# Kernel tuning notes

Hardware: AMD Instinct MI355X
Metric: run time of the kernel (lower is better)

The kernel has to match this reference:

```python
import jax, jax.numpy as jnp
import numpy as np

N, C, H = 4096, 1024, 16
HD = C // H            # 64
DR = HD // 8           # 8 rope freqs per spatial axis


def setup_inputs() -> dict:
    key = jax.random.key(0)
    k1, k2, k3, k4, k5, k6 = jax.random.split(key, 6)
    x = jax.random.normal(k1, (N, C), dtype=jnp.float32)
    coords = jax.random.randint(k2, (N, 5), 0, 64, dtype=jnp.int32)  # [batch, t, h, w, z]
    w_qkv = jax.random.normal(k3, (3 * C, C), dtype=jnp.float32) / np.sqrt(C)
    w_out = jax.random.normal(k4, (C, C), dtype=jnp.float32) / np.sqrt(C)
    gamma_q = jnp.ones((H, HD), dtype=jnp.float32)
    gamma_k = jnp.ones((H, HD), dtype=jnp.float32)
    return {"x": x, "coords": coords, "w_qkv": w_qkv, "w_out": w_out,
            "gamma_q": gamma_q, "gamma_k": gamma_k}


def _rms_norm(t, gamma):
    # F.normalize(dim=-1) * gamma * sqrt(head_dim), computed in fp32
    t = t.astype(jnp.float32)
    nrm = jnp.linalg.norm(t, axis=-1, keepdims=True)
    return t / jnp.maximum(nrm, 1e-12) * gamma * np.float32(np.sqrt(HD))


def _rope_angles(coords):
    # freqs = 1/10000^(arange(DR)/HD); angles per axis (t,h,w,z), concat -> [N, 4*DR] = [N, HD/2]
    freqs = 1.0 / (10000.0 ** (jnp.arange(DR, dtype=jnp.float32) / HD))
    pos = coords[:, 1:].astype(jnp.float32)  # [N,4]
    ang = pos[:, :, None] * freqs[None, None, :]  # [N,4,DR]
    return ang.reshape(ang.shape[0], -1)  # [N, HD/2]


def _apply_rope(t, cos, sin):
    # t: [N,H,HD]; pairs (2i, 2i+1) rotated by angle[i]
    t2 = t.astype(jnp.float32).reshape(t.shape[0], t.shape[1], -1, 2)
    re = t2[..., 0] * cos - t2[..., 1] * sin
    im = t2[..., 0] * sin + t2[..., 1] * cos
    return jnp.stack([re, im], axis=-1).reshape(t.shape)


def reference(x, coords, w_qkv, w_out, gamma_q, gamma_k):
    n = x.shape[0]
    qkv = (x @ w_qkv.T).reshape(n, 3, H, HD)
    q, k, v = qkv[:, 0], qkv[:, 1], qkv[:, 2]  # [N,H,HD]
    q = _rms_norm(q, gamma_q)
    k = _rms_norm(k, gamma_k)
    ang = _rope_angles(coords)              # [N, HD/2]
    cos = jnp.cos(ang)[:, None, :]          # [N,1,HD/2] (broadcast over heads)
    sin = jnp.sin(ang)[:, None, :]
    q = _apply_rope(q, cos, sin)
    k = _apply_rope(k, cos, sin)
    scale = np.float32(1.0 / np.sqrt(HD))
    scores = jnp.einsum('nhd,mhd->hnm', q, k) * scale  # [H,N,N]
    attn = jax.nn.softmax(scores, axis=-1)
    out = jnp.einsum('hnm,mhd->nhd', attn, v).reshape(n, C)
    return out @ w_out.T
```

## Files before the change

kernel.cpp:

```cpp
#include <hip/hip_runtime.h>
#include <hip/hip_bf16.h>

typedef _Float16 half8 __attribute__((ext_vector_type(8)));
typedef _Float16 half4v __attribute__((ext_vector_type(4)));
typedef _Float16 half2 __attribute__((ext_vector_type(2)));
typedef float f32x4 __attribute__((ext_vector_type(4)));

constexpr int NT = 4096;
constexpr int CH = 1024;
constexpr int NH = 16;
constexpr int HD = 64;
constexpr int C3 = 3072;

#if __has_builtin(__builtin_amdgcn_exp2f)
#define EXP2(x) __builtin_amdgcn_exp2f(x)
#else
#define EXP2(x) exp2f(x)
#endif

#define GLOAD_LDS16(gp, lp) __builtin_amdgcn_global_load_lds( \
    (const __attribute__((address_space(1))) void*)(gp),      \
    (__attribute__((address_space(3))) void*)(lp), 16, 0, 0)

static __device__ inline half2 pk_f16(float a, float b) {
  auto r = __builtin_amdgcn_cvt_pkrtz(a, b);
  return *(half2*)&r;
}

__global__ __launch_bounds__(256) void cvt_kernel(const float* __restrict__ in,
                                                  _Float16* __restrict__ out, int n4) {
  int i = blockIdx.x * 256 + threadIdx.x;
  if (i >= n4) return;
  float4 v = ((const float4*)in)[i];
  half4v h;
  h[0] = (_Float16)v.x; h[1] = (_Float16)v.y; h[2] = (_Float16)v.z; h[3] = (_Float16)v.w;
  ((half4v*)out)[i] = h;
}

template <typename OutT>
__global__ __launch_bounds__(256) void gemm_bt(const _Float16* __restrict__ A,
                                               const _Float16* __restrict__ Bt,
                                               OutT* __restrict__ Cc,
                                               int M, int Nn, int K) {
  __shared__ _Float16 As[2][128][32];
  __shared__ _Float16 Bs[2][128][32];
  const int tid = threadIdx.x;
  const int lane = tid & 63, w = tid >> 6;
  const int l15 = lane & 15, l4 = lane >> 4;
  const int m0 = blockIdx.x * 128, n0 = blockIdx.y * 128;
  const int wr = w >> 1, wc = w & 1;
  const int rb = w * 32;
  const int rl = lane >> 2;
  const int cb = (lane & 3) * 8;
  f32x4 acc[4][4] = {};
  auto stage = [&](int k0, int buf) {
    GLOAD_LDS16(A  + (size_t)(m0 + rb + rl) * K + k0 + cb,      &As[buf][rb][0]);
    GLOAD_LDS16(A  + (size_t)(m0 + rb + 16 + rl) * K + k0 + cb, &As[buf][rb + 16][0]);
    GLOAD_LDS16(Bt + (size_t)(n0 + rb + rl) * K + k0 + cb,      &Bs[buf][rb][0]);
    GLOAD_LDS16(Bt + (size_t)(n0 + rb + 16 + rl) * K + k0 + cb, &Bs[buf][rb + 16][0]);
  };
  auto compute = [&](int buf) {
    half8 af[4], bf[4];
#pragma unroll
    for (int mt = 0; mt < 4; ++mt) af[mt] = *(half8*)&As[buf][wr * 64 + mt * 16 + l15][l4 * 8];
#pragma unroll
    for (int nt = 0; nt < 4; ++nt) bf[nt] = *(half8*)&Bs[buf][wc * 64 + nt * 16 + l15][l4 * 8];
#pragma unroll
    for (int mt = 0; mt < 4; ++mt)
#pragma unroll
      for (int nt = 0; nt < 4; ++nt)
        acc[mt][nt] = __builtin_amdgcn_mfma_f32_16x16x32_f16(af[mt], bf[nt], acc[mt][nt], 0, 0, 0);
  };
  stage(0, 0);
  __syncthreads();
  for (int k0 = 0; k0 < K; k0 += 64) {
    stage(k0 + 32, 1);
    compute(0);
    __syncthreads();
    if (k0 + 64 < K) stage(k0 + 64, 0);
    compute(1);
    __syncthreads();
  }
#pragma unroll
  for (int mt = 0; mt < 4; ++mt)
#pragma unroll
    for (int nt = 0; nt < 4; ++nt)
#pragma unroll
      for (int r = 0; r < 4; ++r) {
        int row = m0 + wr * 64 + mt * 16 + l4 * 4 + r;
        int col = n0 + wc * 64 + nt * 16 + l15;
        Cc[(size_t)row * Nn + col] = (OutT)acc[mt][nt][r];
      }
}

__global__ __launch_bounds__(256) void rmsrope_kernel(const _Float16* __restrict__ qkv,
                                                      const int* __restrict__ coords,
                                                      const float* __restrict__ gq,
                                                      const float* __restrict__ gk,
                                                      _Float16* __restrict__ Qh,
                                                      _Float16* __restrict__ KF) {
  int gw = blockIdx.x * 4 + (threadIdx.x >> 6);
  int lane = threadIdx.x & 63;
  int n = gw >> 4, h = gw & 15;
  float q = (float)qkv[(size_t)n * C3 + h * HD + lane];
  float k = (float)qkv[(size_t)n * C3 + CH + h * HD + lane];
  float sq = q * q, sk = k * k;
#pragma unroll
  for (int m = 1; m < 64; m <<= 1) { sq += __shfl_xor(sq, m); sk += __shfl_xor(sk, m); }
  q *= 8.0f / fmaxf(sqrtf(sq), 1e-12f) * gq[h * HD + lane];
  k *= 8.0f / fmaxf(sqrtf(sk), 1e-12f) * gk[h * HD + lane];
  int j = lane >> 1, p = j >> 3, dr = j & 7;
  float ang = (float)coords[n * 5 + 1 + p] * __expf(-(float)dr * 0.14391157f);
  float cs = cosf(ang), sn = sinf(ang);
  float qp = __shfl_xor(q, 1), kp = __shfl_xor(k, 1);
  float qr, kr;
  if ((lane & 1) == 0) { qr = q * cs - qp * sn; kr = k * cs - kp * sn; }
  else                 { qr = qp * sn + q * cs; kr = kp * sn + k * cs; }
  Qh[((size_t)h * NT + n) * HD + lane] = (_Float16)(qr * 0.18033688f);
  int m64 = n & 63, kb = n >> 6;
  int t   = 2 * (m64 >> 5) + ((m64 >> 2) & 1);
  int i15 = 4 * ((m64 >> 3) & 3) + (m64 & 3);
  int kk = lane >> 5, ll4 = (lane >> 3) & 3, jj = lane & 7;
  KF[(size_t)h * NT * HD + (size_t)kb * 4096 +
     (size_t)(((t * 2 + kk) * 64 + ll4 * 16 + i15) * 8 + jj)] = (_Float16)kr;
}

__global__ __launch_bounds__(256) void vtrans_kernel(const _Float16* __restrict__ qkv,
                                                     _Float16* __restrict__ VF) {
  __shared__ _Float16 L[64][72];
  int h = blockIdx.y, n0 = blockIdx.x * 64, kb = blockIdx.x, t0 = threadIdx.x;
#pragma unroll
  for (int i = 0; i < 2; ++i) {
    int cid = t0 + i * 256, r = cid >> 3, c = cid & 7;
    *(half8*)&L[r][c * 8] = *(const half8*)(qkv + (size_t)(n0 + r) * C3 + 2 * CH + h * HD + c * 8);
  }
  __syncthreads();
#pragma unroll
  for (int i = 0; i < 2; ++i) {
    int cid = t0 + i * 256, d = cid >> 3, c = cid & 7;
    half8 v;
#pragma unroll
    for (int jj = 0; jj < 8; ++jj) v[jj] = L[c * 8 + jj][d];
    size_t flat = (size_t)h * NT * HD + (size_t)kb * 4096 +
                  (size_t)((((d >> 4) * 2 + (c >> 2)) * 64 + (c & 3) * 16 + (d & 15)) * 8);
    *(half8*)(VF + flat) = v;
  }
}

__global__ __launch_bounds__(256, 2) void attn_kernel(const _Float16* __restrict__ Qh,
                                                      const _Float16* __restrict__ KF,
                                                      const _Float16* __restrict__ VF,
                                                      _Float16* __restrict__ Oh) {
  __shared__ _Float16 KB[2][4096];
  __shared__ _Float16 VB[2][4096];
  const int tid = threadIdx.x, lane = tid & 63, w = tid >> 6;
  const int l15 = lane & 15, l4 = lane >> 4;
  int bid = blockIdx.x;
  int s = bid >> 3;
  int h = (bid & 7) * 2 + (s >> 5);
  int n0 = (s & 31) * 128;
  half8 qf[2][2];
#pragma unroll
  for (int qb = 0; qb < 2; ++qb)
#pragma unroll
    for (int kk = 0; kk < 2; ++kk)
      qf[qb][kk] = *(const half8*)(Qh + ((size_t)h * NT + n0 + w * 32 + qb * 16 + l15) * HD + kk * 32 + l4 * 8);
  f32x4 acc[2][4] = {};
  f32x4 acc5[2] = {};
  half8 of1 = {};
  if (l15 == 0) {
#pragma unroll
    for (int jq = 0; jq < 8; ++jq) of1[jq] = (_Float16)1.0f;
  }
  const _Float16* KFh = KF + (size_t)h * NT * HD + w * 512 + lane * 8;
  const _Float16* VFh = VF + (size_t)h * NT * HD + w * 512 + lane * 8;
  union U { half8 v; half2 p[4]; };
  auto stage = [&](int kb, int buf) {
    size_t g0 = (size_t)kb * 4096;
    GLOAD_LDS16(KFh + g0,        &KB[buf][w * 512]);
    GLOAD_LDS16(KFh + g0 + 2048, &KB[buf][2048 + w * 512]);
    GLOAD_LDS16(VFh + g0,        &VB[buf][w * 512]);
    GLOAD_LDS16(VFh + g0 + 2048, &VB[buf][2048 + w * 512]);
  };
  auto compute = [&](int buf) {
    f32x4 sv[2][4] = {};
    __builtin_amdgcn_s_setprio(1);
#pragma unroll
    for (int t = 0; t < 4; ++t)
#pragma unroll
      for (int kk = 0; kk < 2; ++kk) {
        half8 kf = *(half8*)&KB[buf][(t * 2 + kk) * 512 + lane * 8];
        sv[0][t] = __builtin_amdgcn_mfma_f32_16x16x32_f16(kf, qf[0][kk], sv[0][t], 0, 0, 0);
        sv[1][t] = __builtin_amdgcn_mfma_f32_16x16x32_f16(kf, qf[1][kk], sv[1][t], 0, 0, 0);
      }
    __builtin_amdgcn_s_setprio(0);
    U u[2][2];
#pragma unroll
    for (int qb = 0; qb < 2; ++qb) {
      float e[4][4];
#pragma unroll
      for (int t = 0; t < 4; ++t)
#pragma unroll
        for (int r = 0; r < 4; ++r) e[t][r] = EXP2(sv[qb][t][r]);
      u[qb][0].p[0] = pk_f16(e[0][0], e[0][1]); u[qb][0].p[1] = pk_f16(e[0][2], e[0][3]);
      u[qb][0].p[2] = pk_f16(e[1][0], e[1][1]); u[qb][0].p[3] = pk_f16(e[1][2], e[1][3]);
      u[qb][1].p[0] = pk_f16(e[2][0], e[2][1]); u[qb][1].p[1] = pk_f16(e[2][2], e[2][3]);
      u[qb][1].p[2] = pk_f16(e[3][0], e[3][1]); u[qb][1].p[3] = pk_f16(e[3][2], e[3][3]);
    }
    __builtin_amdgcn_s_setprio(1);
#pragma unroll
    for (int t = 0; t < 4; ++t)
#pragma unroll
      for (int kk = 0; kk < 2; ++kk) {
        half8 vf = *(half8*)&VB[buf][(t * 2 + kk) * 512 + lane * 8];
        acc[0][t] = __builtin_amdgcn_mfma_f32_16x16x32_f16(u[0][kk].v, vf, acc[0][t], 0, 0, 0);
        acc[1][t] = __builtin_amdgcn_mfma_f32_16x16x32_f16(u[1][kk].v, vf, acc[1][t], 0, 0, 0);
      }
    acc5[0] = __builtin_amdgcn_mfma_f32_16x16x32_f16(u[0][0].v, of1, acc5[0], 0, 0, 0);
    acc5[0] = __builtin_amdgcn_mfma_f32_16x16x32_f16(u[0][1].v, of1, acc5[0], 0, 0, 0);
    acc5[1] = __builtin_amdgcn_mfma_f32_16x16x32_f16(u[1][0].v, of1, acc5[1], 0, 0, 0);
    acc5[1] = __builtin_amdgcn_mfma_f32_16x16x32_f16(u[1][1].v, of1, acc5[1], 0, 0, 0);
    __builtin_amdgcn_s_setprio(0);
  };
  stage(0, 0);
  __syncthreads();
  for (int kb = 0; kb < 64; kb += 2) {
    stage(kb + 1, 1);
    compute(0);
    __syncthreads();
    if (kb + 2 < 64) stage(kb + 2, 0);
    compute(1);
    __syncthreads();
  }
#pragma unroll
  for (int qb = 0; qb < 2; ++qb) {
    float linv[4];
#pragma unroll
    for (int r = 0; r < 4; ++r) linv[r] = 1.0f / __shfl(acc5[qb][r], lane & 48);
#pragma unroll
    for (int t = 0; t < 4; ++t)
#pragma unroll
      for (int r = 0; r < 4; ++r) {
        int row = n0 + w * 32 + qb * 16 + l4 * 4 + r;
        Oh[(size_t)row * CH + h * HD + t * 16 + l15] = (_Float16)(acc[qb][t][r] * linv[r]);
      }
  }
}

extern "C" void kernel_launch(void* const* d_in, const int* in_sizes, int n_in,
                              void* d_out, int out_size, void* d_ws, size_t ws_size,
                              hipStream_t stream) {
  const float* x      = (const float*)d_in[0];
  const int*   coords = (const int*)d_in[1];
  const float* w_qkv  = (const float*)d_in[2];
  const float* w_out  = (const float*)d_in[3];
  const float* gq     = (const float*)d_in[4];
  const float* gk     = (const float*)d_in[5];
  float* out = (float*)d_out;

  char* ws = (char*)d_ws;
  size_t off = 0;
  auto alloc = [&](size_t bytes) { char* p = ws + off; off += bytes; return p; };
  _Float16* xh   = (_Float16*)alloc((size_t)NT * CH * 2);
  _Float16* wqh  = (_Float16*)alloc((size_t)C3 * CH * 2);
  _Float16* woh  = (_Float16*)alloc((size_t)CH * CH * 2);
  _Float16* qkvh = (_Float16*)alloc((size_t)NT * C3 * 2);
  _Float16* Qh   = (_Float16*)alloc((size_t)NT * CH * 2);
  _Float16* KFh  = (_Float16*)alloc((size_t)NT * CH * 2);
  _Float16* VFh  = (_Float16*)alloc((size_t)NT * CH * 2);
  _Float16* Oh   = (_Float16*)alloc((size_t)NT * CH * 2);
  if (off > ws_size) return;

  cvt_kernel<<<NT * CH / 4 / 256, 256, 0, stream>>>(x, xh, NT * CH / 4);
  cvt_kernel<<<C3 * CH / 4 / 256, 256, 0, stream>>>(w_qkv, wqh, C3 * CH / 4);
  cvt_kernel<<<CH * CH / 4 / 256, 256, 0, stream>>>(w_out, woh, CH * CH / 4);
  gemm_bt<_Float16><<<dim3(NT / 128, C3 / 128), 256, 0, stream>>>(xh, wqh, qkvh, NT, C3, CH);
  rmsrope_kernel<<<NT * NH / 4, 256, 0, stream>>>(qkvh, coords, gq, gk, Qh, KFh);
  vtrans_kernel<<<dim3(NT / 64, NH), 256, 0, stream>>>(qkvh, VFh);
  attn_kernel<<<NH * (NT / 128), 256, 0, stream>>>(Qh, KFh, VFh, Oh);
  gemm_bt<float><<<dim3(NT / 128, CH / 128), 256, 0, stream>>>(Oh, woh, out, NT, CH, CH);
}
```

Measured before the change: 177.6 us.

## Fuse conversions, remap GEMM blocks across XCDs, widen attention per-wave query tile

The three fp32-to-fp16 conversion launches are merged into one kernel. Both GEMMs switch to a 1D grid whose block IDs are remapped so consecutive tiles land on the same XCD, aiming at better L2 reuse. The attention kernel drops to 128 threads with 2 waves, and each wave now handles 64 query rows instead of 32, so every K/V fragment read from LDS feeds twice as many MFMAs. This raises register pressure (launch bounds 128,1) and halves the waves per block, which risks lower latency hiding and occupancy.

```diff
diff --git a/kernel.cpp b/kernel.cpp
--- a/kernel.cpp
+++ b/kernel.cpp
@@ -27,27 +27,37 @@
   return *(half2*)&r;
 }
 
-__global__ __launch_bounds__(256) void cvt_kernel(const float* __restrict__ in,
-                                                  _Float16* __restrict__ out, int n4) {
+__global__ __launch_bounds__(256) void cvt3_kernel(const float* __restrict__ a, int na4,
+                                                   const float* __restrict__ b, int nb4,
+                                                   const float* __restrict__ c, int nc4,
+                                                   _Float16* __restrict__ oa,
+                                                   _Float16* __restrict__ ob,
+                                                   _Float16* __restrict__ oc) {
   int i = blockIdx.x * 256 + threadIdx.x;
-  if (i >= n4) return;
-  float4 v = ((const float4*)in)[i];
+  const float* src; _Float16* dst; int j = i;
+  if (i < na4) { src = a; dst = oa; }
+  else if (i < na4 + nb4) { src = b; dst = ob; j = i - na4; }
+  else if (i < na4 + nb4 + nc4) { src = c; dst = oc; j = i - na4 - nb4; }
+  else return;
+  float4 v = ((const float4*)src)[j];
   half4v h;
   h[0] = (_Float16)v.x; h[1] = (_Float16)v.y; h[2] = (_Float16)v.z; h[3] = (_Float16)v.w;
-  ((half4v*)out)[i] = h;
+  ((half4v*)dst)[j] = h;
 }
 
 template <typename OutT>
 __global__ __launch_bounds__(256) void gemm_bt(const _Float16* __restrict__ A,
                                                const _Float16* __restrict__ Bt,
                                                OutT* __restrict__ Cc,
-                                               int M, int Nn, int K) {
+                                               int M, int Nn, int K, int nbx) {
   __shared__ _Float16 As[2][128][32];
   __shared__ _Float16 Bs[2][128][32];
   const int tid = threadIdx.x;
   const int lane = tid & 63, w = tid >> 6;
   const int l15 = lane & 15, l4 = lane >> 4;
-  const int m0 = blockIdx.x * 128, n0 = blockIdx.y * 128;
+  int nwg = gridDim.x, cpx = nwg >> 3;
+  int wg = (blockIdx.x & 7) * cpx + (blockIdx.x >> 3);
+  const int m0 = (wg % nbx) * 128, n0 = (wg / nbx) * 128;
   const int wr = w >> 1, wc = w & 1;
   const int rb = w * 32;
   const int rl = lane >> 2;
@@ -147,7 +157,7 @@
   }
 }
 
-__global__ __launch_bounds__(256, 2) void attn_kernel(const _Float16* __restrict__ Qh,
+__global__ __launch_bounds__(128, 1) void attn_kernel(const _Float16* __restrict__ Qh,
                                                       const _Float16* __restrict__ KF,
                                                       const _Float16* __restrict__ VF,
                                                       _Float16* __restrict__ Oh) {
@@ -159,44 +169,46 @@
   int s = bid >> 3;
   int h = (bid & 7) * 2 + (s >> 5);
   int n0 = (s & 31) * 128;
-  half8 qf[2][2];
-#pragma unroll
-  for (int qb = 0; qb < 2; ++qb)
+  half8 qf[4][2];
+#pragma unroll
+  for (int qb = 0; qb < 4; ++qb)
 #pragma unroll
     for (int kk = 0; kk < 2; ++kk)
-      qf[qb][kk] = *(const half8*)(Qh + ((size_t)h * NT + n0 + w * 32 + qb * 16 + l15) * HD + kk * 32 + l4 * 8);
-  f32x4 acc[2][4] = {};
-  f32x4 acc5[2] = {};
+      qf[qb][kk] = *(const half8*)(Qh + ((size_t)h * NT + n0 + w * 64 + qb * 16 + l15) * HD + kk * 32 + l4 * 8);
+  f32x4 acc[4][4] = {};
+  f32x4 acc5[4] = {};
   half8 of1 = {};
   if (l15 == 0) {
 #pragma unroll
     for (int jq = 0; jq < 8; ++jq) of1[jq] = (_Float16)1.0f;
   }
-  const _Float16* KFh = KF + (size_t)h * NT * HD + w * 512 + lane * 8;
-  const _Float16* VFh = VF + (size_t)h * NT * HD + w * 512 + lane * 8;
+  const _Float16* KFh = KF + (size_t)h * NT * HD + w * 2048 + lane * 8;
+  const _Float16* VFh = VF + (size_t)h * NT * HD + w * 2048 + lane * 8;
   union U { half8 v; half2 p[4]; };
   auto stage = [&](int kb, int buf) {
     size_t g0 = (size_t)kb * 4096;
-    GLOAD_LDS16(KFh + g0,        &KB[buf][w * 512]);
-    GLOAD_LDS16(KFh + g0 + 2048, &KB[buf][2048 + w * 512]);
-    GLOAD_LDS16(VFh + g0,        &VB[buf][w * 512]);
-    GLOAD_LDS16(VFh + g0 + 2048, &VB[buf][2048 + w * 512]);
+#pragma unroll
+    for (int g = 0; g < 4; ++g) {
+      GLOAD_LDS16(KFh + g0 + g * 512, &KB[buf][w * 2048 + g * 512]);
+      GLOAD_LDS16(VFh + g0 + g * 512, &VB[buf][w * 2048 + g * 512]);
+    }
   };
   auto compute = [&](int buf) {
-    f32x4 sv[2][4] = {};
+    f32x4 sv[4][4] = {};
     __builtin_amdgcn_s_setprio(1);
 #pragma unroll
     for (int t = 0; t < 4; ++t)
 #pragma unroll
       for (int kk = 0; kk < 2; ++kk) {
         half8 kf = *(half8*)&KB[buf][(t * 2 + kk) * 512 + lane * 8];
-        sv[0][t] = __builtin_amdgcn_mfma_f32_16x16x32_f16(kf, qf[0][kk], sv[0][t], 0, 0, 0);
-        sv[1][t] = __builtin_amdgcn_mfma_f32_16x16x32_f16(kf, qf[1][kk], sv[1][t], 0, 0, 0);
+#pragma unroll
+        for (int qb = 0; qb < 4; ++qb)
+          sv[qb][t] = __builtin_amdgcn_mfma_f32_16x16x32_f16(kf, qf[qb][kk], sv[qb][t], 0, 0, 0);
       }
     __builtin_amdgcn_s_setprio(0);
-    U u[2][2];
-#pragma unroll
-    for (int qb = 0; qb < 2; ++qb) {
+    U u[4][2];
+#pragma unroll
+    for (int qb = 0; qb < 4; ++qb) {
       float e[4][4];
 #pragma unroll
       for (int t = 0; t < 4; ++t)
@@ -213,13 +225,15 @@
 #pragma unroll
       for (int kk = 0; kk < 2; ++kk) {
         half8 vf = *(half8*)&VB[buf][(t * 2 + kk) * 512 + lane * 8];
-        acc[0][t] = __builtin_amdgcn_mfma_f32_16x16x32_f16(u[0][kk].v, vf, acc[0][t], 0, 0, 0);
-        acc[1][t] = __builtin_amdgcn_mfma_f32_16x16x32_f16(u[1][kk].v, vf, acc[1][t], 0, 0, 0);
-      }
-    acc5[0] = __builtin_amdgcn_mfma_f32_16x16x32_f16(u[0][0].v, of1, acc5[0], 0, 0, 0);
-    acc5[0] = __builtin_amdgcn_mfma_f32_16x16x32_f16(u[0][1].v, of1, acc5[0], 0, 0, 0);
-    acc5[1] = __builtin_amdgcn_mfma_f32_16x16x32_f16(u[1][0].v, of1, acc5[1], 0, 0, 0);
-    acc5[1] = __builtin_amdgcn_mfma_f32_16x16x32_f16(u[1][1].v, of1, acc5[1], 0, 0, 0);
+#pragma unroll
+        for (int qb = 0; qb < 4; ++qb)
+          acc[qb][t] = __builtin_amdgcn_mfma_f32_16x16x32_f16(u[qb][kk].v, vf, acc[qb][t], 0, 0, 0);
+      }
+#pragma unroll
+    for (int qb = 0; qb < 4; ++qb) {
+      acc5[qb] = __builtin_amdgcn_mfma_f32_16x16x32_f16(u[qb][0].v, of1, acc5[qb], 0, 0, 0);
+      acc5[qb] = __builtin_amdgcn_mfma_f32_16x16x32_f16(u[qb][1].v, of1, acc5[qb], 0, 0, 0);
+    }
     __builtin_amdgcn_s_setprio(0);
   };
   stage(0, 0);
@@ -233,7 +247,7 @@
     __syncthreads();
   }
 #pragma unroll
-  for (int qb = 0; qb < 2; ++qb) {
+  for (int qb = 0; qb < 4; ++qb) {
     float linv[4];
 #pragma unroll
     for (int r = 0; r < 4; ++r) linv[r] = 1.0f / __shfl(acc5[qb][r], lane & 48);
@@ -241,7 +255,7 @@
     for (int t = 0; t < 4; ++t)
 #pragma unroll
       for (int r = 0; r < 4; ++r) {
-        int row = n0 + w * 32 + qb * 16 + l4 * 4 + r;
+        int row = n0 + w * 64 + qb * 16 + l4 * 4 + r;
         Oh[(size_t)row * CH + h * HD + t * 16 + l15] = (_Float16)(acc[qb][t][r] * linv[r]);
       }
   }
@@ -271,12 +285,12 @@
   _Float16* Oh   = (_Float16*)alloc((size_t)NT * CH * 2);
   if (off > ws_size) return;
 
-  cvt_kernel<<<NT * CH / 4 / 256, 256, 0, stream>>>(x, xh, NT * CH / 4);
-  cvt_kernel<<<C3 * CH / 4 / 256, 256, 0, stream>>>(w_qkv, wqh, C3 * CH / 4);
-  cvt_kernel<<<CH * CH / 4 / 256, 256, 0, stream>>>(w_out, woh, CH * CH / 4);
-  gemm_bt<_Float16><<<dim3(NT / 128, C3 / 128), 256, 0, stream>>>(xh, wqh, qkvh, NT, C3, CH);
+  int na4 = NT * CH / 4, nb4 = C3 * CH / 4, nc4 = CH * CH / 4;
+  cvt3_kernel<<<(na4 + nb4 + nc4) / 256, 256, 0, stream>>>(x, na4, w_qkv, nb4, w_out, nc4,
+                                                           xh, wqh, woh);
+  gemm_bt<_Float16><<<(NT / 128) * (C3 / 128), 256, 0, stream>>>(xh, wqh, qkvh, NT, C3, CH, NT / 128);
   rmsrope_kernel<<<NT * NH / 4, 256, 0, stream>>>(qkvh, coords, gq, gk, Qh, KFh);
   vtrans_kernel<<<dim3(NT / 64, NH), 256, 0, stream>>>(qkvh, VFh);
-  attn_kernel<<<NH * (NT / 128), 256, 0, stream>>>(Qh, KFh, VFh, Oh);
-  gemm_bt<float><<<dim3(NT / 128, CH / 128), 256, 0, stream>>>(Oh, woh, out, NT, CH, CH);
-}
+  attn_kernel<<<NH * (NT / 128), 128, 0, stream>>>(Qh, KFh, VFh, Oh);
+  gemm_bt<float><<<(NT / 128) * (CH / 128), 256, 0, stream>>>(Oh, woh, out, NT, CH, CH, NT / 128);
+}
```

After: 196.8 us. 10.8% more time.

## Add 256x256 fragment-layout QKV GEMM, XCD-swizzle blocks, single-buffer attention

Applied to the files above, without the earlier changes.

Converts x and w_qkv into a pre-tiled fragment layout so a new 512-thread 256x256-tile GEMM can stage whole K-tiles with direct global-to-LDS loads and interleave prefetch with MFMA phases. It also remaps workgroup IDs so neighbouring tiles land on the same XCD, in both GEMMs. The attention kernel drops its K/V double buffer for a single buffer with two barriers per step, which lowers LDS use but exposes load latency. The new GEMM requests 128KB of dynamic LDS at two blocks per CU, which depends on the LDS capacity available.

```diff
diff --git a/kernel.cpp b/kernel.cpp
--- a/kernel.cpp
+++ b/kernel.cpp
@@ -37,17 +37,117 @@
   ((half4v*)out)[i] = h;
 }
 
+__global__ __launch_bounds__(256) void cvt_frag_kernel(const float* __restrict__ in,
+                                                       _Float16* __restrict__ out,
+                                                       int n4, int Kd) {
+  int i = blockIdx.x * 256 + threadIdx.x;
+  if (i >= n4) return;
+  int kq = Kd >> 2;
+  int r = i / kq, k = (i - r * kq) * 4;
+  float4 v = ((const float4*)in)[i];
+  int bt = r >> 8, rr = r & 255;
+  int kt = k >> 6, kr = k & 63;
+  int frag = ((rr >> 4) << 1) + (kr >> 5);
+  size_t flat = (((size_t)bt * (Kd >> 6) + kt) * 32 + frag) * 512
+              + ((((kr >> 3) & 3) * 16 + (rr & 15)) << 3) + (kr & 7);
+  half4v h;
+  h[0] = (_Float16)v.x; h[1] = (_Float16)v.y; h[2] = (_Float16)v.z; h[3] = (_Float16)v.w;
+  *(half4v*)(out + flat) = h;
+}
+
+__global__ __launch_bounds__(512, 2) void gemm8p(const _Float16* __restrict__ A2,
+                                                 const _Float16* __restrict__ B2,
+                                                 _Float16* __restrict__ Cc,
+                                                 int M, int Nn, int K, int nbx) {
+  extern __shared__ _Float16 lds[];
+  const int tid = threadIdx.x;
+  const int lane = tid & 63, w = tid >> 6;
+  const int l15 = lane & 15, l4 = lane >> 4;
+  const int wr = w >> 2, wc = w & 3;
+  int nwg = gridDim.x, cpx = nwg >> 3;
+  int wg = (blockIdx.x & 7) * cpx + (blockIdx.x >> 3);
+  const int bm = wg % nbx, bn = wg / nbx;
+  const int ktiles = K >> 6;
+  const _Float16* Abase = A2 + (size_t)bm * ktiles * 16384 + tid * 8;
+  const _Float16* Bbase = B2 + (size_t)bn * ktiles * 16384 + tid * 8;
+  f32x4 acc[8][4] = {};
+  auto stageA = [&](int kt, int buf) {
+    const _Float16* s = Abase + (size_t)kt * 16384;
+    _Float16* d = lds + buf * 16384 + tid * 8;
+#pragma unroll
+    for (int i = 0; i < 4; ++i) GLOAD_LDS16(s + i * 4096, d + i * 4096);
+  };
+  auto stageB = [&](int kt, int buf) {
+    const _Float16* s = Bbase + (size_t)kt * 16384;
+    _Float16* d = lds + 32768 + buf * 16384 + tid * 8;
+#pragma unroll
+    for (int i = 0; i < 4; ++i) GLOAD_LDS16(s + i * 4096, d + i * 4096);
+  };
+  stageA(0, 0);
+  stageB(0, 0);
+  for (int kt = 0; kt < ktiles; ++kt) {
+    const int cur = kt & 1, nxt = cur ^ 1;
+    const _Float16* Ac = lds + cur * 16384 + lane * 8;
+    const _Float16* Bc = lds + 32768 + cur * 16384 + lane * 8;
+    asm volatile("s_waitcnt vmcnt(0)" ::: "memory");
+    __builtin_amdgcn_sched_barrier(0);
+    __builtin_amdgcn_s_barrier();
+    __builtin_amdgcn_sched_barrier(0);
+#pragma unroll
+    for (int ph = 0; ph < 4; ++ph) {
+      const int mh = ph >> 1, nh = ph & 1;
+      half8 af[4][2], bf[2][2];
+#pragma unroll
+      for (int mt = 0; mt < 4; ++mt)
+#pragma unroll
+        for (int kk = 0; kk < 2; ++kk)
+          af[mt][kk] = *(half8*)(Ac + ((((wr * 8 + mh * 4 + mt) << 1) + kk) << 9));
+#pragma unroll
+      for (int nt = 0; nt < 2; ++nt)
+#pragma unroll
+        for (int kk = 0; kk < 2; ++kk)
+          bf[nt][kk] = *(half8*)(Bc + ((((wc * 4 + nh * 2 + nt) << 1) + kk) << 9));
+      if (ph == 0 && kt + 1 < ktiles) stageA(kt + 1, nxt);
+      if (ph == 1 && kt + 1 < ktiles) stageB(kt + 1, nxt);
+      __builtin_amdgcn_s_barrier();
+      __builtin_amdgcn_s_setprio(1);
+#pragma unroll
+      for (int mt = 0; mt < 4; ++mt)
+#pragma unroll
+        for (int nt = 0; nt < 2; ++nt)
+#pragma unroll
+          for (int kk = 0; kk < 2; ++kk)
+            acc[mh * 4 + mt][nh * 2 + nt] = __builtin_amdgcn_mfma_f32_16x16x32_f16(
+                af[mt][kk], bf[nt][kk], acc[mh * 4 + mt][nh * 2 + nt], 0, 0, 0);
+      __builtin_amdgcn_s_setprio(0);
+      __builtin_amdgcn_s_barrier();
+    }
+  }
+#pragma unroll
+  for (int mt8 = 0; mt8 < 8; ++mt8)
+#pragma unroll
+    for (int nt4 = 0; nt4 < 4; ++nt4)
+#pragma unroll
+      for (int r = 0; r < 4; ++r) {
+        int row = bm * 256 + wr * 128 + mt8 * 16 + l4 * 4 + r;
+        int col = bn * 256 + wc * 64 + nt4 * 16 + l15;
+        Cc[(size_t)row * Nn + col] = (_Float16)acc[mt8][nt4][r];
+      }
+}
+
 template <typename OutT>
 __global__ __launch_bounds__(256) void gemm_bt(const _Float16* __restrict__ A,
                                                const _Float16* __restrict__ Bt,
                                                OutT* __restrict__ Cc,
-                                               int M, int Nn, int K) {
+                                               int M, int Nn, int K, int nbx) {
   __shared__ _Float16 As[2][128][32];
   __shared__ _Float16 Bs[2][128][32];
   const int tid = threadIdx.x;
   const int lane = tid & 63, w = tid >> 6;
   const int l15 = lane & 15, l4 = lane >> 4;
-  const int m0 = blockIdx.x * 128, n0 = blockIdx.y * 128;
+  int nwg = gridDim.x, cpx = nwg >> 3;
+  int wg = (blockIdx.x & 7) * cpx + (blockIdx.x >> 3);
+  const int m0 = (wg % nbx) * 128, n0 = (wg / nbx) * 128;
   const int wr = w >> 1, wc = w & 1;
   const int rb = w * 32;
   const int rl = lane >> 2;
@@ -151,8 +251,8 @@
                                                       const _Float16* __restrict__ KF,
                                                       const _Float16* __restrict__ VF,
                                                       _Float16* __restrict__ Oh) {
-  __shared__ _Float16 KB[2][4096];
-  __shared__ _Float16 VB[2][4096];
+  __shared__ _Float16 KB[4096];
+  __shared__ _Float16 VB[4096];
   const int tid = threadIdx.x, lane = tid & 63, w = tid >> 6;
   const int l15 = lane & 15, l4 = lane >> 4;
   int bid = blockIdx.x;
@@ -175,21 +275,23 @@
   const _Float16* KFh = KF + (size_t)h * NT * HD + w * 512 + lane * 8;
   const _Float16* VFh = VF + (size_t)h * NT * HD + w * 512 + lane * 8;
   union U { half8 v; half2 p[4]; };
-  auto stage = [&](int kb, int buf) {
-    size_t g0 = (size_t)kb * 4096;
-    GLOAD_LDS16(KFh + g0,        &KB[buf][w * 512]);
-    GLOAD_LDS16(KFh + g0 + 2048, &KB[buf][2048 + w * 512]);
-    GLOAD_LDS16(VFh + g0,        &VB[buf][w * 512]);
-    GLOAD_LDS16(VFh + g0 + 2048, &VB[buf][2048 + w * 512]);
-  };
-  auto compute = [&](int buf) {
+  for (int kb = 0; kb < 64; ++kb) {
+    __syncthreads();
+    {
+      size_t g0 = (size_t)kb * 4096;
+      GLOAD_LDS16(KFh + g0,        &KB[w * 512]);
+      GLOAD_LDS16(KFh + g0 + 2048, &KB[2048 + w * 512]);
+      GLOAD_LDS16(VFh + g0,        &VB[w * 512]);
+      GLOAD_LDS16(VFh + g0 + 2048, &VB[2048 + w * 512]);
+    }
+    __syncthreads();
     f32x4 sv[2][4] = {};
     __builtin_amdgcn_s_setprio(1);
 #pragma unroll
     for (int t = 0; t < 4; ++t)
 #pragma unroll
       for (int kk = 0; kk < 2; ++kk) {
-        half8 kf = *(half8*)&KB[buf][(t * 2 + kk) * 512 + lane * 8];
+        half8 kf = *(half8*)&KB[(t * 2 + kk) * 512 + lane * 8];
         sv[0][t] = __builtin_amdgcn_mfma_f32_16x16x32_f16(kf, qf[0][kk], sv[0][t], 0, 0, 0);
         sv[1][t] = __builtin_amdgcn_mfma_f32_16x16x32_f16(kf, qf[1][kk], sv[1][t], 0, 0, 0);
       }
@@ -212,7 +314,7 @@
     for (int t = 0; t < 4; ++t)
 #pragma unroll
       for (int kk = 0; kk < 2; ++kk) {
-        half8 vf = *(half8*)&VB[buf][(t * 2 + kk) * 512 + lane * 8];
+        half8 vf = *(half8*)&VB[(t * 2 + kk) * 512 + lane * 8];
         acc[0][t] = __builtin_amdgcn_mfma_f32_16x16x32_f16(u[0][kk].v, vf, acc[0][t], 0, 0, 0);
         acc[1][t] = __builtin_amdgcn_mfma_f32_16x16x32_f16(u[1][kk].v, vf, acc[1][t], 0, 0, 0);
       }
@@ -221,16 +323,6 @@
     acc5[1] = __builtin_amdgcn_mfma_f32_16x16x32_f16(u[1][0].v, of1, acc5[1], 0, 0, 0);
     acc5[1] = __builtin_amdgcn_mfma_f32_16x16x32_f16(u[1][1].v, of1, acc5[1], 0, 0, 0);
     __builtin_amdgcn_s_setprio(0);
-  };
-  stage(0, 0);
-  __syncthreads();
-  for (int kb = 0; kb < 64; kb += 2) {
-    stage(kb + 1, 1);
-    compute(0);
-    __syncthreads();
-    if (kb + 2 < 64) stage(kb + 2, 0);
-    compute(1);
-    __syncthreads();
   }
 #pragma unroll
   for (int qb = 0; qb < 2; ++qb) {
@@ -271,12 +363,12 @@
   _Float16* Oh   = (_Float16*)alloc((size_t)NT * CH * 2);
   if (off > ws_size) return;
 
-  cvt_kernel<<<NT * CH / 4 / 256, 256, 0, stream>>>(x, xh, NT * CH / 4);
-  cvt_kernel<<<C3 * CH / 4 / 256, 256, 0, stream>>>(w_qkv, wqh, C3 * CH / 4);
+  cvt_frag_kernel<<<NT * CH / 4 / 256, 256, 0, stream>>>(x, xh, NT * CH / 4, CH);
+  cvt_frag_kernel<<<C3 * CH / 4 / 256, 256, 0, stream>>>(w_qkv, wqh, C3 * CH / 4, CH);
   cvt_kernel<<<CH * CH / 4 / 256, 256, 0, stream>>>(w_out, woh, CH * CH / 4);
-  gemm_bt<_Float16><<<dim3(NT / 128, C3 / 128), 256, 0, stream>>>(xh, wqh, qkvh, NT, C3, CH);
+  gemm8p<<<(NT / 256) * (C3 / 256), 512, 131072, stream>>>(xh, wqh, qkvh, NT, C3, CH, NT / 256);
   rmsrope_kernel<<<NT * NH / 4, 256, 0, stream>>>(qkvh, coords, gq, gk, Qh, KFh);
   vtrans_kernel<<<dim3(NT / 64, NH), 256, 0, stream>>>(qkvh, VFh);
   attn_kernel<<<NH * (NT / 128), 256, 0, stream>>>(Qh, KFh, VFh, Oh);
-  gemm_bt<float><<<dim3(NT / 128, CH / 128), 256, 0, stream>>>(Oh, woh, out, NT, CH, CH);
-}
+  gemm_bt<float><<<(NT / 128) * (CH / 128), 256, 0, stream>>>(Oh, woh, out, NT, CH, CH, NT / 128);
+}
```

After: 182.9 us. +2.9%, slower.

## Fuse RMSNorm, RoPE and K/V relayout into QKV GEMM epilogue; merge conversion kernels

Applied to the files above, without the earlier changes.

Folds the RMS normalisation, rotary embedding and the K/V fragment relayout into the epilogue of the QKV projection GEMM, staging through LDS, so the intermediate fp16 QKV buffer and two extra kernels go away. The three fp32→fp16 conversions become one launch, and RoPE cos/sin come from a small precomputed table. Both GEMMs now remap workgroup IDs so consecutive blocks land on the same XCD. The attention kernel drops its K/V double buffering for a single buffer with two barriers per step, which frees LDS but removes load/compute overlap.

```diff
diff --git a/kernel.cpp b/kernel.cpp
--- a/kernel.cpp
+++ b/kernel.cpp
@@ -27,27 +27,50 @@
   return *(half2*)&r;
 }
 
-__global__ __launch_bounds__(256) void cvt_kernel(const float* __restrict__ in,
-                                                  _Float16* __restrict__ out, int n4) {
+__global__ __launch_bounds__(256) void cvt3_kernel(const float* __restrict__ a, int na4,
+                                                   const float* __restrict__ b, int nb4,
+                                                   const float* __restrict__ c, int nc4,
+                                                   _Float16* __restrict__ oa,
+                                                   _Float16* __restrict__ ob,
+                                                   _Float16* __restrict__ oc) {
   int i = blockIdx.x * 256 + threadIdx.x;
-  if (i >= n4) return;
-  float4 v = ((const float4*)in)[i];
+  const float* src; _Float16* dst; int j = i;
+  if (i < na4) { src = a; dst = oa; }
+  else if (i < na4 + nb4) { src = b; dst = ob; j = i - na4; }
+  else if (i < na4 + nb4 + nc4) { src = c; dst = oc; j = i - na4 - nb4; }
+  else return;
+  float4 v = ((const float4*)src)[j];
   half4v h;
   h[0] = (_Float16)v.x; h[1] = (_Float16)v.y; h[2] = (_Float16)v.z; h[3] = (_Float16)v.w;
-  ((half4v*)out)[i] = h;
-}
-
-template <typename OutT>
-__global__ __launch_bounds__(256) void gemm_bt(const _Float16* __restrict__ A,
-                                               const _Float16* __restrict__ Bt,
-                                               OutT* __restrict__ Cc,
-                                               int M, int Nn, int K) {
-  __shared__ _Float16 As[2][128][32];
-  __shared__ _Float16 Bs[2][128][32];
+  ((half4v*)dst)[j] = h;
+}
+
+__global__ __launch_bounds__(256) void rope_tab_kernel(const int* __restrict__ coords,
+                                                       float2* __restrict__ csn) {
+  int idx = blockIdx.x * 256 + threadIdx.x;
+  int n = idx >> 5, j = idx & 31;
+  float ang = (float)coords[n * 5 + 1 + (j >> 3)] * __expf(-(float)(j & 7) * 0.14391157f);
+  csn[idx] = make_float2(cosf(ang), sinf(ang));
+}
+
+__global__ __launch_bounds__(256) void gemm_qkv(const _Float16* __restrict__ A,
+                                                const _Float16* __restrict__ Bt,
+                                                const float2* __restrict__ csn,
+                                                const float* __restrict__ gq,
+                                                const float* __restrict__ gk,
+                                                _Float16* __restrict__ Qh,
+                                                _Float16* __restrict__ KF,
+                                                _Float16* __restrict__ VF) {
+  __shared__ __align__(16) char smem[36864];
+  auto As = (_Float16(*)[128][32])smem;
+  auto Bs = (_Float16(*)[128][32])(smem + 16384);
+  const int K = CH, Nn = C3, nbx = NT / 128;
   const int tid = threadIdx.x;
   const int lane = tid & 63, w = tid >> 6;
   const int l15 = lane & 15, l4 = lane >> 4;
-  const int m0 = blockIdx.x * 128, n0 = blockIdx.y * 128;
+  int nwg = gridDim.x, cpx = nwg >> 3;
+  int wg = (blockIdx.x & 7) * cpx + (blockIdx.x >> 3);
+  const int m0 = (wg % nbx) * 128, n0 = (wg / nbx) * 128;
   const int wr = w >> 1, wc = w & 1;
   const int rb = w * 32;
   const int rl = lane >> 2;
@@ -81,6 +104,128 @@
     compute(1);
     __syncthreads();
   }
+  const int gc0 = n0 + wc * 64;
+  const int sec = gc0 >> 10;
+  const int h   = (gc0 & 1023) >> 6;
+  const int K0  = m0 + wr * 64;
+  _Float16* Lw = (_Float16*)(smem + w * 9216);
+  if (sec < 2) {
+    const float* gm = (sec == 0) ? gq : gk;
+    float gmm[4];
+#pragma unroll
+    for (int nt = 0; nt < 4; ++nt) gmm[nt] = gm[h * 64 + nt * 16 + l15];
+    const float qsc = (sec == 0) ? 0.18033688f : 1.0f;
+#pragma unroll
+    for (int mt = 0; mt < 4; ++mt)
+#pragma unroll
+      for (int r = 0; r < 4; ++r) {
+        float ss = 0.f;
+#pragma unroll
+        for (int nt = 0; nt < 4; ++nt) ss += acc[mt][nt][r] * acc[mt][nt][r];
+        ss += __shfl_xor(ss, 1); ss += __shfl_xor(ss, 2);
+        ss += __shfl_xor(ss, 4); ss += __shfl_xor(ss, 8);
+        float sc = 8.0f / fmaxf(sqrtf(ss), 1e-12f);
+        int row = mt * 16 + l4 * 4 + r;
+        int n = K0 + row;
+#pragma unroll
+        for (int nt = 0; nt < 4; ++nt) {
+          float v = acc[mt][nt][r] * sc * gmm[nt];
+          float2 cz = csn[n * 32 + nt * 8 + (l15 >> 1)];
+          float p = __shfl_xor(v, 1);
+          float o = ((l15 & 1) == 0) ? (v * cz.x - p * cz.y) : (p * cz.y + v * cz.x);
+          Lw[row * 72 + nt * 16 + l15] = (_Float16)(o * qsc);
+        }
+      }
+  } else {
+#pragma unroll
+    for (int mt = 0; mt < 4; ++mt)
+#pragma unroll
+      for (int r = 0; r < 4; ++r) {
+        int row = mt * 16 + l4 * 4 + r;
+#pragma unroll
+        for (int nt = 0; nt < 4; ++nt)
+          Lw[row * 72 + nt * 16 + l15] = (_Float16)acc[mt][nt][r];
+      }
+  }
+  const int kb = K0 >> 6;
+  if (sec == 0) {
+#pragma unroll
+    for (int i = 0; i < 8; ++i) {
+      int row = i * 8 + (lane >> 3), col = (lane & 7) * 8;
+      half8 vv = *(half8*)&Lw[row * 72 + col];
+      *(half8*)(Qh + ((size_t)h * NT + K0 + row) * 64 + col) = vv;
+    }
+  } else if (sec == 1) {
+    _Float16* base = KF + (size_t)h * NT * HD + (size_t)kb * 4096;
+#pragma unroll
+    for (int i = 0; i < 8; ++i) {
+      int t = i >> 1, kk = i & 1;
+      int i15 = lane & 15, ll4 = lane >> 4;
+      int m = ((t >> 1) << 5) | ((i15 >> 2) << 3) | ((t & 1) << 2) | (i15 & 3);
+      half8 vv = *(half8*)&Lw[m * 72 + kk * 32 + ll4 * 8];
+      *(half8*)(base + (size_t)(((t * 2 + kk) * 64 + ll4 * 16 + i15) * 8)) = vv;
+    }
+  } else {
+    _Float16* base = VF + (size_t)h * NT * HD + (size_t)kb * 4096;
+#pragma unroll
+    for (int i = 0; i < 8; ++i) {
+      int t = i >> 1, kk = i & 1;
+      int l15v = lane & 15, l4v = lane >> 4;
+      half8 vv;
+#pragma unroll
+      for (int jj = 0; jj < 8; ++jj)
+        vv[jj] = Lw[(kk * 32 + l4v * 8 + jj) * 72 + t * 16 + l15v];
+      *(half8*)(base + (size_t)(((t * 2 + kk) * 64 + l4v * 16 + l15v) * 8)) = vv;
+    }
+  }
+}
+
+template <typename OutT>
+__global__ __launch_bounds__(256) void gemm_bt(const _Float16* __restrict__ A,
+                                               const _Float16* __restrict__ Bt,
+                                               OutT* __restrict__ Cc,
+                                               int M, int Nn, int K, int nbx) {
+  __shared__ _Float16 As[2][128][32];
+  __shared__ _Float16 Bs[2][128][32];
+  const int tid = threadIdx.x;
+  const int lane = tid & 63, w = tid >> 6;
+  const int l15 = lane & 15, l4 = lane >> 4;
+  int nwg = gridDim.x, cpx = nwg >> 3;
+  int wg = (blockIdx.x & 7) * cpx + (blockIdx.x >> 3);
+  const int m0 = (wg % nbx) * 128, n0 = (wg / nbx) * 128;
+  const int wr = w >> 1, wc = w & 1;
+  const int rb = w * 32;
+  const int rl = lane >> 2;
+  const int cb = (lane & 3) * 8;
+  f32x4 acc[4][4] = {};
+  auto stage = [&](int k0, int buf) {
+    GLOAD_LDS16(A  + (size_t)(m0 + rb + rl) * K + k0 + cb,      &As[buf][rb][0]);
+    GLOAD_LDS16(A  + (size_t)(m0 + rb + 16 + rl) * K + k0 + cb, &As[buf][rb + 16][0]);
+    GLOAD_LDS16(Bt + (size_t)(n0 + rb + rl) * K + k0 + cb,      &Bs[buf][rb][0]);
+    GLOAD_LDS16(Bt + (size_t)(n0 + rb + 16 + rl) * K + k0 + cb, &Bs[buf][rb + 16][0]);
+  };
+  auto compute = [&](int buf) {
+    half8 af[4], bf[4];
+#pragma unroll
+    for (int mt = 0; mt < 4; ++mt) af[mt] = *(half8*)&As[buf][wr * 64 + mt * 16 + l15][l4 * 8];
+#pragma unroll
+    for (int nt = 0; nt < 4; ++nt) bf[nt] = *(half8*)&Bs[buf][wc * 64 + nt * 16 + l15][l4 * 8];
+#pragma unroll
+    for (int mt = 0; mt < 4; ++mt)
+#pragma unroll
+      for (int nt = 0; nt < 4; ++nt)
+        acc[mt][nt] = __builtin_amdgcn_mfma_f32_16x16x32_f16(af[mt], bf[nt], acc[mt][nt], 0, 0, 0);
+  };
+  stage(0, 0);
+  __syncthreads();
+  for (int k0 = 0; k0 < K; k0 += 64) {
+    stage(k0 + 32, 1);
+    compute(0);
+    __syncthreads();
+    if (k0 + 64 < K) stage(k0 + 64, 0);
+    compute(1);
+    __syncthreads();
+  }
 #pragma unroll
   for (int mt = 0; mt < 4; ++mt)
 #pragma unroll
@@ -93,66 +238,12 @@
       }
 }
 
-__global__ __launch_bounds__(256) void rmsrope_kernel(const _Float16* __restrict__ qkv,
-                                                      const int* __restrict__ coords,
-                                                      const float* __restrict__ gq,
-                                                      const float* __restrict__ gk,
-                                                      _Float16* __restrict__ Qh,
-                                                      _Float16* __restrict__ KF) {
-  int gw = blockIdx.x * 4 + (threadIdx.x >> 6);
-  int lane = threadIdx.x & 63;
-  int n = gw >> 4, h = gw & 15;
-  float q = (float)qkv[(size_t)n * C3 + h * HD + lane];
-  float k = (float)qkv[(size_t)n * C3 + CH + h * HD + lane];
-  float sq = q * q, sk = k * k;
-#pragma unroll
-  for (int m = 1; m < 64; m <<= 1) { sq += __shfl_xor(sq, m); sk += __shfl_xor(sk, m); }
-  q *= 8.0f / fmaxf(sqrtf(sq), 1e-12f) * gq[h * HD + lane];
-  k *= 8.0f / fmaxf(sqrtf(sk), 1e-12f) * gk[h * HD + lane];
-  int j = lane >> 1, p = j >> 3, dr = j & 7;
-  float ang = (float)coords[n * 5 + 1 + p] * __expf(-(float)dr * 0.14391157f);
-  float cs = cosf(ang), sn = sinf(ang);
-  float qp = __shfl_xor(q, 1), kp = __shfl_xor(k, 1);
-  float qr, kr;
-  if ((lane & 1) == 0) { qr = q * cs - qp * sn; kr = k * cs - kp * sn; }
-  else                 { qr = qp * sn + q * cs; kr = kp * sn + k * cs; }
-  Qh[((size_t)h * NT + n) * HD + lane] = (_Float16)(qr * 0.18033688f);
-  int m64 = n & 63, kb = n >> 6;
-  int t   = 2 * (m64 >> 5) + ((m64 >> 2) & 1);
-  int i15 = 4 * ((m64 >> 3) & 3) + (m64 & 3);
-  int kk = lane >> 5, ll4 = (lane >> 3) & 3, jj = lane & 7;
-  KF[(size_t)h * NT * HD + (size_t)kb * 4096 +
-     (size_t)(((t * 2 + kk) * 64 + ll4 * 16 + i15) * 8 + jj)] = (_Float16)kr;
-}
-
-__global__ __launch_bounds__(256) void vtrans_kernel(const _Float16* __restrict__ qkv,
-                                                     _Float16* __restrict__ VF) {
-  __shared__ _Float16 L[64][72];
-  int h = blockIdx.y, n0 = blockIdx.x * 64, kb = blockIdx.x, t0 = threadIdx.x;
-#pragma unroll
-  for (int i = 0; i < 2; ++i) {
-    int cid = t0 + i * 256, r = cid >> 3, c = cid & 7;
-    *(half8*)&L[r][c * 8] = *(const half8*)(qkv + (size_t)(n0 + r) * C3 + 2 * CH + h * HD + c * 8);
-  }
-  __syncthreads();
-#pragma unroll
-  for (int i = 0; i < 2; ++i) {
-    int cid = t0 + i * 256, d = cid >> 3, c = cid & 7;
-    half8 v;
-#pragma unroll
-    for (int jj = 0; jj < 8; ++jj) v[jj] = L[c * 8 + jj][d];
-    size_t flat = (size_t)h * NT * HD + (size_t)kb * 4096 +
-                  (size_t)((((d >> 4) * 2 + (c >> 2)) * 64 + (c & 3) * 16 + (d & 15)) * 8);
-    *(half8*)(VF + flat) = v;
-  }
-}
-
 __global__ __launch_bounds__(256, 2) void attn_kernel(const _Float16* __restrict__ Qh,
                                                       const _Float16* __restrict__ KF,
                                                       const _Float16* __restrict__ VF,
                                                       _Float16* __restrict__ Oh) {
-  __shared__ _Float16 KB[2][4096];
-  __shared__ _Float16 VB[2][4096];
+  __shared__ _Float16 KB[4096];
+  __shared__ _Float16 VB[4096];
   const int tid = threadIdx.x, lane = tid & 63, w = tid >> 6;
   const int l15 = lane & 15, l4 = lane >> 4;
   int bid = blockIdx.x;
@@ -175,21 +266,23 @@
   const _Float16* KFh = KF + (size_t)h * NT * HD + w * 512 + lane * 8;
   const _Float16* VFh = VF + (size_t)h * NT * HD + w * 512 + lane * 8;
   union U { half8 v; half2 p[4]; };
-  auto stage = [&](int kb, int buf) {
-    size_t g0 = (size_t)kb * 4096;
-    GLOAD_LDS16(KFh + g0,        &KB[buf][w * 512]);
-    GLOAD_LDS16(KFh + g0 + 2048, &KB[buf][2048 + w * 512]);
-    GLOAD_LDS16(VFh + g0,        &VB[buf][w * 512]);
-    GLOAD_LDS16(VFh + g0 + 2048, &VB[buf][2048 + w * 512]);
-  };
-  auto compute = [&](int buf) {
+  for (int kb = 0; kb < 64; ++kb) {
+    __syncthreads();
+    {
+      size_t g0 = (size_t)kb * 4096;
+      GLOAD_LDS16(KFh + g0,        &KB[w * 512]);
+      GLOAD_LDS16(KFh + g0 + 2048, &KB[2048 + w * 512]);
+      GLOAD_LDS16(VFh + g0,        &VB[w * 512]);
+      GLOAD_LDS16(VFh + g0 + 2048, &VB[2048 + w * 512]);
+    }
+    __syncthreads();
     f32x4 sv[2][4] = {};
     __builtin_amdgcn_s_setprio(1);
 #pragma unroll
     for (int t = 0; t < 4; ++t)
 #pragma unroll
       for (int kk = 0; kk < 2; ++kk) {
-        half8 kf = *(half8*)&KB[buf][(t * 2 + kk) * 512 + lane * 8];
+        half8 kf = *(half8*)&KB[(t * 2 + kk) * 512 + lane * 8];
         sv[0][t] = __builtin_amdgcn_mfma_f32_16x16x32_f16(kf, qf[0][kk], sv[0][t], 0, 0, 0);
         sv[1][t] = __builtin_amdgcn_mfma_f32_16x16x32_f16(kf, qf[1][kk], sv[1][t], 0, 0, 0);
       }
@@ -212,7 +305,7 @@
     for (int t = 0; t < 4; ++t)
 #pragma unroll
       for (int kk = 0; kk < 2; ++kk) {
-        half8 vf = *(half8*)&VB[buf][(t * 2 + kk) * 512 + lane * 8];
+        half8 vf = *(half8*)&VB[(t * 2 + kk) * 512 + lane * 8];
         acc[0][t] = __builtin_amdgcn_mfma_f32_16x16x32_f16(u[0][kk].v, vf, acc[0][t], 0, 0, 0);
         acc[1][t] = __builtin_amdgcn_mfma_f32_16x16x32_f16(u[1][kk].v, vf, acc[1][t], 0, 0, 0);
       }
@@ -221,16 +314,6 @@
     acc5[1] = __builtin_amdgcn_mfma_f32_16x16x32_f16(u[1][0].v, of1, acc5[1], 0, 0, 0);
     acc5[1] = __builtin_amdgcn_mfma_f32_16x16x32_f16(u[1][1].v, of1, acc5[1], 0, 0, 0);
     __builtin_amdgcn_s_setprio(0);
-  };
-  stage(0, 0);
-  __syncthreads();
-  for (int kb = 0; kb < 64; kb += 2) {
-    stage(kb + 1, 1);
-    compute(0);
-    __syncthreads();
-    if (kb + 2 < 64) stage(kb + 2, 0);
-    compute(1);
-    __syncthreads();
   }
 #pragma unroll
   for (int qb = 0; qb < 2; ++qb) {
@@ -264,19 +347,18 @@
   _Float16* xh   = (_Float16*)alloc((size_t)NT * CH * 2);
   _Float16* wqh  = (_Float16*)alloc((size_t)C3 * CH * 2);
   _Float16* woh  = (_Float16*)alloc((size_t)CH * CH * 2);
-  _Float16* qkvh = (_Float16*)alloc((size_t)NT * C3 * 2);
+  float2*   csn  = (float2*)alloc((size_t)NT * 32 * 8);
   _Float16* Qh   = (_Float16*)alloc((size_t)NT * CH * 2);
   _Float16* KFh  = (_Float16*)alloc((size_t)NT * CH * 2);
   _Float16* VFh  = (_Float16*)alloc((size_t)NT * CH * 2);
   _Float16* Oh   = (_Float16*)alloc((size_t)NT * CH * 2);
   if (off > ws_size) return;
 
-  cvt_kernel<<<NT * CH / 4 / 256, 256, 0, stream>>>(x, xh, NT * CH / 4);
-  cvt_kernel<<<C3 * CH / 4 / 256, 256, 0, stream>>>(w_qkv, wqh, C3 * CH / 4);
-  cvt_kernel<<<CH * CH / 4 / 256, 256, 0, stream>>>(w_out, woh, CH * CH / 4);
-  gemm_bt<_Float16><<<dim3(NT / 128, C3 / 128), 256, 0, stream>>>(xh, wqh, qkvh, NT, C3, CH);
-  rmsrope_kernel<<<NT * NH / 4, 256, 0, stream>>>(qkvh, coords, gq, gk, Qh, KFh);
-  vtrans_kernel<<<dim3(NT / 64, NH), 256, 0, stream>>>(qkvh, VFh);
+  int na4 = NT * CH / 4, nb4 = C3 * CH / 4, nc4 = CH * CH / 4;
+  cvt3_kernel<<<(na4 + nb4 + nc4) / 256, 256, 0, stream>>>(x, na4, w_qkv, nb4, w_out, nc4,
+                                                           xh, wqh, woh);
+  rope_tab_kernel<<<NT * 32 / 256, 256, 0, stream>>>(coords, csn);
+  gemm_qkv<<<(NT / 128) * (C3 / 128), 256, 0, stream>>>(xh, wqh, csn, gq, gk, Qh, KFh, VFh);
   attn_kernel<<<NH * (NT / 128), 256, 0, stream>>>(Qh, KFh, VFh, Oh);
-  gemm_bt<float><<<dim3(NT / 128, CH / 128), 256, 0, stream>>>(Oh, woh, out, NT, CH, CH);
-}
+  gemm_bt<float><<<(NT / 128) * (CH / 128), 256, 0, stream>>>(Oh, woh, out, NT, CH, CH, NT / 128);
+}
```

New measurement: 163.9 us. 1.08x faster.
